# Kernel optimization log

Measured on AMD Instinct MI355X. Metric: run time of the kernel, lower is better.

The kernel has to match this reference:

```python
import jax, jax.numpy as jnp
import numpy as np

N = 50000      # nodes
E = 1600000    # edges (avg degree 32)
DIN, DH, DOUT = 256, 128, 64


def gcn_conv(x, W, b, row, col, w, n):
    """One GCNConv layer (self-loops already appended to row/col/w).
    row = source nodes, col = target nodes; aggregate at targets."""
    xw = x @ W                                        # [n, d_out]
    deg = jax.ops.segment_sum(w, col, num_segments=n)  # in-degree weighted
    dinv = jnp.where(deg > 0, jax.lax.rsqrt(deg), 0.0)
    norm = dinv[row] * w * dinv[col]                  # [E+n]
    msg = norm[:, None] * xw[row]                     # [E+n, d_out] gather
    out = jax.ops.segment_sum(msg, col, num_segments=n)
    return out + b


def setup_inputs() -> dict:
    key = jax.random.key(0)
    k = jax.random.split(key, 6)
    x = jax.random.normal(k[0], (N, DIN), dtype=jnp.float32)
    edge_index = jax.random.randint(k[1], (2, E), 0, N)
    edge_weight = jax.random.uniform(k[2], (E,), dtype=jnp.float32)
    W1 = jax.random.normal(k[3], (DIN, DH), dtype=jnp.float32) * (1.0 / np.sqrt(DIN))
    b1 = jnp.zeros((DH,), dtype=jnp.float32)
    W2 = jax.random.normal(k[4], (DH, DOUT), dtype=jnp.float32) * (1.0 / np.sqrt(DH))
    b2 = jnp.zeros((DOUT,), dtype=jnp.float32)
    return {"x": x, "edge_index": edge_index, "edge_weight": edge_weight,
            "W1": W1, "b1": b1, "W2": W2, "b2": b2}


def reference(x, edge_index, edge_weight, W1, b1, W2, b2):
    n = x.shape[0]
    loops = jnp.arange(n, dtype=edge_index.dtype)
    row = jnp.concatenate([edge_index[0], loops])
    col = jnp.concatenate([edge_index[1], loops])
    w = jnp.concatenate([edge_weight, jnp.ones((n,), dtype=edge_weight.dtype)])
    h = gcn_conv(x, W1, b1, row, col, w, n)
    h = jax.nn.relu(h)
    # dropout(p=0.2) is identity in eval mode
    h = gcn_conv(h, W2, b2, row, col, w, n)
    return jax.nn.log_softmax(h, axis=-1)
```

## Files before the change

kernel.cpp:

```cpp
#include <hip/hip_runtime.h>
#include <hip/hip_bf16.h>
#include <cstddef>


#define DIN 256
#define DH  128
#define DOUT 64
#define NPB 100
#define NBMAX 512

typedef __bf16 bf16x8 __attribute__((ext_vector_type(8)));
typedef float f32x4 __attribute__((ext_vector_type(4)));

__device__ __forceinline__ float bflo(unsigned u) { return __uint_as_float(u << 16); }
__device__ __forceinline__ float bfhi(unsigned u) { return __uint_as_float(u & 0xffff0000u); }
__device__ __forceinline__ unsigned short f2bf(float f) {
    unsigned u = __float_as_uint(f);
    unsigned r = (u + 0x7fffu + ((u >> 16) & 1u)) >> 16;
    return (unsigned short)r;
}

__global__ void prep_w_kernel(const float* __restrict__ W1, const float* __restrict__ W2,
                              unsigned short* __restrict__ wt1, unsigned short* __restrict__ wt2) {
    int i = blockIdx.x * 256 + threadIdx.x;
    if (i < DH * DIN) {
        int nn = i >> 8, k = i & 255;
        wt1[i] = f2bf(W1[k * DH + nn]);
    } else {
        int j = i - DH * DIN;
        if (j < DOUT * DH) {
            int nn = j >> 7, k = j & 127;
            wt2[j] = f2bf(W2[k * DOUT + nn]);
        }
    }
}

__launch_bounds__(256)
__global__ void hist_kernel(const int* __restrict__ col, int* __restrict__ bh,
                            int E, int Ec, int NB) {
    __shared__ int hist[NBMAX];
    int p = blockIdx.x, t = threadIdx.x;
    for (int b = t; b < NB; b += 256) hist[b] = 0;
    __syncthreads();
    int s = p * Ec, e = min(s + Ec, E);
    for (int i = s + t; i < e; i += 256) atomicAdd(&hist[col[i] / NPB], 1);
    __syncthreads();
    for (int b = t; b < NB; b += 256) bh[p * NB + b] = hist[b];
}

__launch_bounds__(512)
__global__ void colscan_kernel(int* __restrict__ bh, int* __restrict__ btotal,
                               int P, int NB) {
    __shared__ int arr[512];
    int b = blockIdx.x, t = threadIdx.x;
    arr[t] = (t < P) ? bh[t * NB + b] : 0;
    __syncthreads();
    for (int off = 1; off < 512; off <<= 1) {
        int v = (t >= off) ? arr[t - off] : 0;
        __syncthreads();
        arr[t] += v;
        __syncthreads();
    }
    int excl = (t == 0) ? 0 : arr[t - 1];
    if (t < P) bh[t * NB + b] = excl;
    if (t == P - 1) btotal[b] = arr[t];
}

__launch_bounds__(512)
__global__ void basescan_kernel(const int* __restrict__ btotal, int* __restrict__ bbase,
                                int* __restrict__ rowptr, int NB, int n, int E) {
    __shared__ int arr[512];
    int t = threadIdx.x;
    arr[t] = (t < NB) ? btotal[t] : 0;
    __syncthreads();
    for (int off = 1; off < 512; off <<= 1) {
        int v = (t >= off) ? arr[t - off] : 0;
        __syncthreads();
        arr[t] += v;
        __syncthreads();
    }
    int excl = (t == 0) ? 0 : arr[t - 1];
    if (t <= NB) bbase[t] = excl;
    if (t == 511) rowptr[n] = E;
}

__launch_bounds__(256)
__global__ void scatter_kernel(const int* __restrict__ row, const int* __restrict__ col,
                               const float* __restrict__ w, const int* __restrict__ bh,
                               const int* __restrict__ bbase, int2* __restrict__ part,
                               int E, int Ec, int NB) {
    __shared__ int cur[NBMAX];
    int p = blockIdx.x, t = threadIdx.x;
    for (int b = t; b < NB; b += 256) cur[b] = bbase[b] + bh[p * NB + b];
    __syncthreads();
    int s = p * Ec, e = min(s + Ec, E);
    for (int i = s + t; i < e; i += 256) {
        int c = col[i];
        int r = row[i];
        int b = c / NPB;
        int pos = atomicAdd(&cur[b], 1);
        part[pos] = make_int2(r | ((c - b * NPB) << 16), __float_as_int(w[i]));
    }
}

__launch_bounds__(256)
__global__ void bucket_csr_kernel(const int2* __restrict__ part, const int* __restrict__ bbase,
                                  float* __restrict__ dinv, int* __restrict__ rowptr,
                                  int2* __restrict__ final_e, int n) {
    __shared__ int   hist[NPB];
    __shared__ float wsum[NPB];
    __shared__ int   nbase[NPB];
    __shared__ int   cur[NPB];
    int b = blockIdx.x, t = threadIdx.x;
    if (t < NPB) { hist[t] = 0; wsum[t] = 0.0f; }
    __syncthreads();
    int s = bbase[b], e = bbase[b + 1];
    for (int i = s + t; i < e; i += 256) {
        int2 rec = part[i];
        int cl = rec.x >> 16;
        atomicAdd(&hist[cl], 1);
        atomicAdd(&wsum[cl], __int_as_float(rec.y));
    }
    __syncthreads();
    if (t == 0) {
        int run = 0;
        for (int k = 0; k < NPB; ++k) { nbase[k] = run; run += hist[k]; }
    }
    __syncthreads();
    if (t < NPB) {
        int node = b * NPB + t;
        if (node < n) {
            dinv[node] = rsqrtf(1.0f + wsum[t]);
            rowptr[node] = s + nbase[t];
        }
        cur[t] = nbase[t];
    }
    __syncthreads();
    for (int i = s + t; i < e; i += 256) {
        int2 rec = part[i];
        int cl = rec.x >> 16;
        int q = s + atomicAdd(&cur[cl], 1);
        final_e[q] = make_int2(rec.x & 0xffff, rec.y);
    }
}

template <int K, int M>
__launch_bounds__(256)
__global__ void gemm_mfma_kernel(const float* __restrict__ A,
                                 const unsigned short* __restrict__ Wt,
                                 const float* __restrict__ scale,
                                 unsigned short* __restrict__ C, int N) {
    constexpr int BK = 64, LD = BK + 8;
    constexpr int WN = M / 4;
    constexpr int NT = WN / 16;
    constexpr int CLD = M + 8;
    constexpr int SM = (64 * LD + M * LD) > (64 * CLD) ? (64 * LD + M * LD) : (64 * CLD);
    __shared__ unsigned short smem[SM];
    __shared__ float sdv[64];
    unsigned short* As = smem;
    unsigned short* Bs = smem + 64 * LD;

    const int tid = threadIdx.x;
    const int row0 = blockIdx.x * 64;
    const int lane = tid & 63;
    const int quad = lane >> 4, r16 = lane & 15;
    const int n0 = (tid >> 6) * WN;

    if (tid < 64) {
        int r = row0 + tid;
        sdv[tid] = (r < N) ? scale[r] : 0.0f;
    }

    f32x4 acc[4][NT];
#pragma unroll
    for (int mt = 0; mt < 4; ++mt)
#pragma unroll
        for (int nt = 0; nt < NT; ++nt)
            acc[mt][nt] = (f32x4){0.f, 0.f, 0.f, 0.f};

    for (int k0 = 0; k0 < K; k0 += BK) {
#pragma unroll
        for (int j = 0; j < 4; ++j) {
            int idx = tid + j * 256;
            int m = idx >> 4;
            int q = idx & 15;
            int gr = row0 + m;
            float4 v = make_float4(0.f, 0.f, 0.f, 0.f);
            if (gr < N) v = *(const float4*)&A[(size_t)gr * K + k0 + q * 4];
            ushort4 s4;
            s4.x = f2bf(v.x); s4.y = f2bf(v.y); s4.z = f2bf(v.z); s4.w = f2bf(v.w);
            *(ushort4*)&As[m * LD + q * 4] = s4;
        }
#pragma unroll
        for (int j = 0; j < M * 8 / 256; ++j) {
            int idx = tid + j * 256;
            int nn = idx >> 3;
            int q = idx & 7;
            uint4 v = *(const uint4*)&Wt[(size_t)nn * K + k0 + q * 8];
            *(uint4*)&Bs[nn * LD + q * 8] = v;
        }
        __syncthreads();
#pragma unroll
        for (int ks = 0; ks < BK / 32; ++ks) {
            bf16x8 af[4], bfr[NT];
#pragma unroll
            for (int nt = 0; nt < NT; ++nt)
                bfr[nt] = *(const bf16x8*)&Bs[(n0 + nt * 16 + r16) * LD + ks * 32 + quad * 8];
#pragma unroll
            for (int mt = 0; mt < 4; ++mt)
                af[mt] = *(const bf16x8*)&As[(mt * 16 + r16) * LD + ks * 32 + quad * 8];
#pragma unroll
            for (int mt = 0; mt < 4; ++mt)
#pragma unroll
                for (int nt = 0; nt < NT; ++nt)
                    acc[mt][nt] = __builtin_amdgcn_mfma_f32_16x16x32_bf16(
                        af[mt], bfr[nt], acc[mt][nt], 0, 0, 0);
        }
        __syncthreads();
    }
    unsigned short* Cs = smem;
#pragma unroll
    for (int mt = 0; mt < 4; ++mt) {
#pragma unroll
        for (int i = 0; i < 4; ++i) {
            int r = mt * 16 + quad * 4 + i;
            float sc = sdv[r];
#pragma unroll
            for (int nt = 0; nt < NT; ++nt)
                Cs[r * CLD + n0 + nt * 16 + r16] = f2bf(acc[mt][nt][i] * sc);
        }
    }
    __syncthreads();
#pragma unroll
    for (int j = 0; j < 64 * M / 8 / 256; ++j) {
        int idx = tid + j * 256;
        int r = idx / (M / 8);
        int q = idx % (M / 8);
        int gr = row0 + r;
        if (gr < N) {
            uint4 v = *(const uint4*)&Cs[r * CLD + q * 8];
            *(uint4*)&C[(size_t)gr * M + q * 8] = v;
        }
    }
}

__launch_bounds__(256)
__global__ void agg1_kernel(const uint2* __restrict__ xw,
                            const int* __restrict__ rowptr,
                            const int2* __restrict__ edge,
                            const float* __restrict__ dinv,
                            const float* __restrict__ bias,
                            float* __restrict__ out, int n) {
    int node = blockIdx.x * 4 + (threadIdx.x >> 6);
    if (node >= n) return;
    int lane = threadIdx.x & 63;
    int half = lane >> 5, sub = lane & 31;
    float a0 = 0.f, a1 = 0.f, a2 = 0.f, a3 = 0.f;
    if (half == 0) {
        uint2 u = xw[(size_t)node * 32 + sub];
        a0 = bflo(u.x); a1 = bfhi(u.x); a2 = bflo(u.y); a3 = bfhi(u.y);
    }
    int p = rowptr[node], p1 = rowptr[node + 1];
    for (; p + 8 <= p1; p += 8) {
        int2 e0 = edge[p + half],     e1 = edge[p + 2 + half];
        int2 e2 = edge[p + 4 + half], e3 = edge[p + 6 + half];
        uint2 v0 = xw[(size_t)e0.x * 32 + sub];
        uint2 v1 = xw[(size_t)e1.x * 32 + sub];
        uint2 v2 = xw[(size_t)e2.x * 32 + sub];
        uint2 v3 = xw[(size_t)e3.x * 32 + sub];
        float w0 = __int_as_float(e0.y), w1 = __int_as_float(e1.y);
        float w2 = __int_as_float(e2.y), w3 = __int_as_float(e3.y);
        a0 += w0 * bflo(v0.x) + w1 * bflo(v1.x) + w2 * bflo(v2.x) + w3 * bflo(v3.x);
        a1 += w0 * bfhi(v0.x) + w1 * bfhi(v1.x) + w2 * bfhi(v2.x) + w3 * bfhi(v3.x);
        a2 += w0 * bflo(v0.y) + w1 * bflo(v1.y) + w2 * bflo(v2.y) + w3 * bflo(v3.y);
        a3 += w0 * bfhi(v0.y) + w1 * bfhi(v1.y) + w2 * bfhi(v2.y) + w3 * bfhi(v3.y);
    }
    for (; p + 2 <= p1; p += 2) {
        int2 e0 = edge[p + half];
        uint2 v0 = xw[(size_t)e0.x * 32 + sub];
        float w0 = __int_as_float(e0.y);
        a0 += w0 * bflo(v0.x); a1 += w0 * bfhi(v0.x);
        a2 += w0 * bflo(v0.y); a3 += w0 * bfhi(v0.y);
    }
    if (p < p1 && half == 0) {
        int2 e0 = edge[p];
        uint2 v0 = xw[(size_t)e0.x * 32 + sub];
        float w0 = __int_as_float(e0.y);
        a0 += w0 * bflo(v0.x); a1 += w0 * bfhi(v0.x);
        a2 += w0 * bflo(v0.y); a3 += w0 * bfhi(v0.y);
    }
    a0 += __shfl_xor(a0, 32); a1 += __shfl_xor(a1, 32);
    a2 += __shfl_xor(a2, 32); a3 += __shfl_xor(a3, 32);
    float di = dinv[node];
    float4 b = ((const float4*)bias)[sub];
    a0 = fmaxf(di * a0 + b.x, 0.f);
    a1 = fmaxf(di * a1 + b.y, 0.f);
    a2 = fmaxf(di * a2 + b.z, 0.f);
    a3 = fmaxf(di * a3 + b.w, 0.f);
    if (half == 0)
        ((float4*)out)[(size_t)node * 32 + sub] = make_float4(a0, a1, a2, a3);
}

__launch_bounds__(256)
__global__ void agg2_kernel(const uint2* __restrict__ xw,
                            const int* __restrict__ rowptr,
                            const int2* __restrict__ edge,
                            const float* __restrict__ dinv,
                            const float* __restrict__ bias,
                            float* __restrict__ out, int n) {
    int node = blockIdx.x * 4 + (threadIdx.x >> 6);
    if (node >= n) return;
    int lane = threadIdx.x & 63;
    int qw = lane >> 4, sub = lane & 15;
    float a0 = 0.f, a1 = 0.f, a2 = 0.f, a3 = 0.f;
    if (qw == 0) {
        uint2 u = xw[(size_t)node * 16 + sub];
        a0 = bflo(u.x); a1 = bfhi(u.x); a2 = bflo(u.y); a3 = bfhi(u.y);
    }
    int p = rowptr[node], p1 = rowptr[node + 1];
    for (; p + 8 <= p1; p += 8) {
        int2 e0 = edge[p + qw], e1 = edge[p + 4 + qw];
        uint2 v0 = xw[(size_t)e0.x * 16 + sub];
        uint2 v1 = xw[(size_t)e1.x * 16 + sub];
        float w0 = __int_as_float(e0.y), w1 = __int_as_float(e1.y);
        a0 += w0 * bflo(v0.x) + w1 * bflo(v1.x);
        a1 += w0 * bfhi(v0.x) + w1 * bfhi(v1.x);
        a2 += w0 * bflo(v0.y) + w1 * bflo(v1.y);
        a3 += w0 * bfhi(v0.y) + w1 * bfhi(v1.y);
    }
    for (; p + 4 <= p1; p += 4) {
        int2 e0 = edge[p + qw];
        uint2 v0 = xw[(size_t)e0.x * 16 + sub];
        float w0 = __int_as_float(e0.y);
        a0 += w0 * bflo(v0.x); a1 += w0 * bfhi(v0.x);
        a2 += w0 * bflo(v0.y); a3 += w0 * bfhi(v0.y);
    }
    int rem = p1 - p;
    if (qw < rem) {
        int2 e0 = edge[p + qw];
        uint2 v0 = xw[(size_t)e0.x * 16 + sub];
        float w0 = __int_as_float(e0.y);
        a0 += w0 * bflo(v0.x); a1 += w0 * bfhi(v0.x);
        a2 += w0 * bflo(v0.y); a3 += w0 * bfhi(v0.y);
    }
    a0 += __shfl_xor(a0, 32); a1 += __shfl_xor(a1, 32);
    a2 += __shfl_xor(a2, 32); a3 += __shfl_xor(a3, 32);
    a0 += __shfl_xor(a0, 16); a1 += __shfl_xor(a1, 16);
    a2 += __shfl_xor(a2, 16); a3 += __shfl_xor(a3, 16);
    float di = dinv[node];
    float4 b = ((const float4*)bias)[sub];
    a0 = di * a0 + b.x; a1 = di * a1 + b.y;
    a2 = di * a2 + b.z; a3 = di * a3 + b.w;
    float m = fmaxf(fmaxf(a0, a1), fmaxf(a2, a3));
#pragma unroll
    for (int off = 8; off > 0; off >>= 1) m = fmaxf(m, __shfl_xor(m, off));
    float s = __expf(a0 - m) + __expf(a1 - m) + __expf(a2 - m) + __expf(a3 - m);
#pragma unroll
    for (int off = 8; off > 0; off >>= 1) s += __shfl_xor(s, off);
    float lse = m + __logf(s);
    if (qw == 0)
        ((float4*)out)[(size_t)node * 16 + sub] =
            make_float4(a0 - lse, a1 - lse, a2 - lse, a3 - lse);
}

extern "C" void kernel_launch(void* const* d_in, const int* in_sizes, int n_in,
                              void* d_out, int out_size, void* d_ws, size_t ws_size,
                              hipStream_t stream) {
    const float* x  = (const float*)d_in[0];
    const int*   ei = (const int*)d_in[1];
    const float* ew = (const float*)d_in[2];
    const float* W1 = (const float*)d_in[3];
    const float* b1 = (const float*)d_in[4];
    const float* W2 = (const float*)d_in[5];
    const float* b2 = (const float*)d_in[6];
    float* out = (float*)d_out;

    const int n = in_sizes[0] / DIN;
    const int E = in_sizes[2];
    const int* row = ei;
    const int* col = ei + E;

    const int NB = (n + NPB - 1) / NPB;
    const int P  = NB;
    const int Ec = (E + P - 1) / P;

    char* ptr = (char*)d_ws;
    auto alloc = [&](size_t bytes) -> void* {
        void* r = (void*)ptr;
        ptr += (bytes + 255) & ~(size_t)255;
        return r;
    };
    int*   bh     = (int*)  alloc((size_t)P * NB * 4);
    int*   btotal = (int*)  alloc((size_t)NB * 4);
    int*   bbase  = (int*)  alloc((size_t)(NB + 1) * 4);
    int*   rowptr = (int*)  alloc((size_t)(n + 1) * 4);
    float* dinv   = (float*)alloc((size_t)n * 4);
    int2*  edge   = (int2*) alloc((size_t)E * 8);
    unsigned short* xw1 = (unsigned short*)alloc((size_t)n * DH * 2);
    unsigned short* wt1 = (unsigned short*)alloc((size_t)DH * DIN * 2);
    unsigned short* wt2 = (unsigned short*)alloc((size_t)DOUT * DH * 2);
    char* tail = (char*)alloc((size_t)n * DH * 4);
    int2*  part = (int2*)tail;
    float* h1   = (float*)tail;
    unsigned short* xw2 = xw1;

    const int nb_g = (n + 63) / 64;
    const int nb_a = (n + 3) / 4;

    prep_w_kernel<<<(DH * DIN + DOUT * DH + 255) / 256, 256, 0, stream>>>(W1, W2, wt1, wt2);
    hist_kernel<<<P, 256, 0, stream>>>(col, bh, E, Ec, NB);
    colscan_kernel<<<NB, 512, 0, stream>>>(bh, btotal, P, NB);
    basescan_kernel<<<1, 512, 0, stream>>>(btotal, bbase, rowptr, NB, n, E);
    scatter_kernel<<<P, 256, 0, stream>>>(row, col, ew, bh, bbase, part, E, Ec, NB);
    bucket_csr_kernel<<<NB, 256, 0, stream>>>(part, bbase, dinv, rowptr, edge, n);

    gemm_mfma_kernel<DIN, DH><<<nb_g, 256, 0, stream>>>(x, wt1, dinv, xw1, n);
    agg1_kernel<<<nb_a, 256, 0, stream>>>((const uint2*)xw1, rowptr, edge, dinv, b1, h1, n);
    gemm_mfma_kernel<DH, DOUT><<<nb_g, 256, 0, stream>>>(h1, wt2, dinv, xw2, n);
    agg2_kernel<<<nb_a, 256, 0, stream>>>((const uint2*)xw2, rowptr, edge, dinv, b2, out, n);
}
```

Measured before the change: 286.6 us.

## Fuse weight prep into histogram, parallel bucket scan, persistent deeper-unrolled aggregation

Merges the weight transpose/bf16 conversion into the histogram kernel as extra blocks, which removes one launch. Replaces the serial single-thread prefix sum in bucket_csr with a block-wide Hillis-Steele scan. Turns both aggregation kernels into grid-stride loops over a fixed 2048-block grid and unrolls the edge loop to 16 edges, so more gathers are in flight per wave. The risks are higher register pressure and some load imbalance from the fixed grid size.

```diff
diff --git a/kernel.cpp b/kernel.cpp
--- a/kernel.cpp
+++ b/kernel.cpp
@@ -20,26 +20,27 @@
     return (unsigned short)r;
 }
 
-__global__ void prep_w_kernel(const float* __restrict__ W1, const float* __restrict__ W2,
-                              unsigned short* __restrict__ wt1, unsigned short* __restrict__ wt2) {
-    int i = blockIdx.x * 256 + threadIdx.x;
-    if (i < DH * DIN) {
-        int nn = i >> 8, k = i & 255;
-        wt1[i] = f2bf(W1[k * DH + nn]);
-    } else {
-        int j = i - DH * DIN;
-        if (j < DOUT * DH) {
-            int nn = j >> 7, k = j & 127;
-            wt2[j] = f2bf(W2[k * DOUT + nn]);
-        }
-    }
-}
-
-__launch_bounds__(256)
-__global__ void hist_kernel(const int* __restrict__ col, int* __restrict__ bh,
-                            int E, int Ec, int NB) {
+__launch_bounds__(256)
+__global__ void hist_prep_kernel(const int* __restrict__ col, int* __restrict__ bh,
+                                 int E, int Ec, int NB, int P,
+                                 const float* __restrict__ W1, const float* __restrict__ W2,
+                                 unsigned short* __restrict__ wt1, unsigned short* __restrict__ wt2) {
     __shared__ int hist[NBMAX];
     int p = blockIdx.x, t = threadIdx.x;
+    if (p >= P) {
+        int i = (p - P) * 256 + t;
+        if (i < DH * DIN) {
+            int nn = i >> 8, k = i & 255;
+            wt1[i] = f2bf(W1[k * DH + nn]);
+        } else {
+            int j = i - DH * DIN;
+            if (j < DOUT * DH) {
+                int nn = j >> 7, k = j & 127;
+                wt2[j] = f2bf(W2[k * DOUT + nn]);
+            }
+        }
+        return;
+    }
     for (int b = t; b < NB; b += 256) hist[b] = 0;
     __syncthreads();
     int s = p * Ec, e = min(s + Ec, E);
@@ -109,6 +110,7 @@
                                   int2* __restrict__ final_e, int n) {
     __shared__ int   hist[NPB];
     __shared__ float wsum[NPB];
+    __shared__ int   arr[256];
     __shared__ int   nbase[NPB];
     __shared__ int   cur[NPB];
     int b = blockIdx.x, t = threadIdx.x;
@@ -122,18 +124,24 @@
         atomicAdd(&wsum[cl], __int_as_float(rec.y));
     }
     __syncthreads();
-    if (t == 0) {
-        int run = 0;
-        for (int k = 0; k < NPB; ++k) { nbase[k] = run; run += hist[k]; }
-    }
-    __syncthreads();
+    int hv = (t < NPB) ? hist[t] : 0;
+    arr[t] = hv;
+    __syncthreads();
+    for (int off = 1; off < 256; off <<= 1) {
+        int v = (t >= off) ? arr[t - off] : 0;
+        __syncthreads();
+        arr[t] += v;
+        __syncthreads();
+    }
     if (t < NPB) {
+        int nb = arr[t] - hv;
+        nbase[t] = nb;
+        cur[t] = nb;
         int node = b * NPB + t;
         if (node < n) {
             dinv[node] = rsqrtf(1.0f + wsum[t]);
-            rowptr[node] = s + nbase[t];
-        }
-        cur[t] = nbase[t];
+            rowptr[node] = s + nb;
+        }
     }
     __syncthreads();
     for (int i = s + t; i < e; i += 256) {
@@ -251,54 +259,55 @@
                             const float* __restrict__ dinv,
                             const float* __restrict__ bias,
                             float* __restrict__ out, int n) {
-    int node = blockIdx.x * 4 + (threadIdx.x >> 6);
-    if (node >= n) return;
-    int lane = threadIdx.x & 63;
-    int half = lane >> 5, sub = lane & 31;
-    float a0 = 0.f, a1 = 0.f, a2 = 0.f, a3 = 0.f;
-    if (half == 0) {
-        uint2 u = xw[(size_t)node * 32 + sub];
-        a0 = bflo(u.x); a1 = bfhi(u.x); a2 = bflo(u.y); a3 = bfhi(u.y);
-    }
-    int p = rowptr[node], p1 = rowptr[node + 1];
-    for (; p + 8 <= p1; p += 8) {
-        int2 e0 = edge[p + half],     e1 = edge[p + 2 + half];
-        int2 e2 = edge[p + 4 + half], e3 = edge[p + 6 + half];
-        uint2 v0 = xw[(size_t)e0.x * 32 + sub];
-        uint2 v1 = xw[(size_t)e1.x * 32 + sub];
-        uint2 v2 = xw[(size_t)e2.x * 32 + sub];
-        uint2 v3 = xw[(size_t)e3.x * 32 + sub];
-        float w0 = __int_as_float(e0.y), w1 = __int_as_float(e1.y);
-        float w2 = __int_as_float(e2.y), w3 = __int_as_float(e3.y);
-        a0 += w0 * bflo(v0.x) + w1 * bflo(v1.x) + w2 * bflo(v2.x) + w3 * bflo(v3.x);
-        a1 += w0 * bfhi(v0.x) + w1 * bfhi(v1.x) + w2 * bfhi(v2.x) + w3 * bfhi(v3.x);
-        a2 += w0 * bflo(v0.y) + w1 * bflo(v1.y) + w2 * bflo(v2.y) + w3 * bflo(v3.y);
-        a3 += w0 * bfhi(v0.y) + w1 * bfhi(v1.y) + w2 * bfhi(v2.y) + w3 * bfhi(v3.y);
-    }
-    for (; p + 2 <= p1; p += 2) {
-        int2 e0 = edge[p + half];
-        uint2 v0 = xw[(size_t)e0.x * 32 + sub];
-        float w0 = __int_as_float(e0.y);
-        a0 += w0 * bflo(v0.x); a1 += w0 * bfhi(v0.x);
-        a2 += w0 * bflo(v0.y); a3 += w0 * bfhi(v0.y);
-    }
-    if (p < p1 && half == 0) {
-        int2 e0 = edge[p];
-        uint2 v0 = xw[(size_t)e0.x * 32 + sub];
-        float w0 = __int_as_float(e0.y);
-        a0 += w0 * bflo(v0.x); a1 += w0 * bfhi(v0.x);
-        a2 += w0 * bflo(v0.y); a3 += w0 * bfhi(v0.y);
-    }
-    a0 += __shfl_xor(a0, 32); a1 += __shfl_xor(a1, 32);
-    a2 += __shfl_xor(a2, 32); a3 += __shfl_xor(a3, 32);
-    float di = dinv[node];
-    float4 b = ((const float4*)bias)[sub];
-    a0 = fmaxf(di * a0 + b.x, 0.f);
-    a1 = fmaxf(di * a1 + b.y, 0.f);
-    a2 = fmaxf(di * a2 + b.z, 0.f);
-    a3 = fmaxf(di * a3 + b.w, 0.f);
-    if (half == 0)
-        ((float4*)out)[(size_t)node * 32 + sub] = make_float4(a0, a1, a2, a3);
+    const int nw = gridDim.x * 4;
+    const int wid = blockIdx.x * 4 + (threadIdx.x >> 6);
+    const int lane = threadIdx.x & 63;
+    const int half = lane >> 5, sub = lane & 31;
+    for (int node = wid; node < n; node += nw) {
+        float a0 = 0.f, a1 = 0.f, a2 = 0.f, a3 = 0.f;
+        if (half == 0) {
+            uint2 u = xw[(size_t)node * 32 + sub];
+            a0 = bflo(u.x); a1 = bfhi(u.x); a2 = bflo(u.y); a3 = bfhi(u.y);
+        }
+        int p = rowptr[node], p1 = rowptr[node + 1];
+        for (; p + 16 <= p1; p += 16) {
+            int2 e[8]; uint2 v[8];
+#pragma unroll
+            for (int j = 0; j < 8; ++j) e[j] = edge[p + 2 * j + half];
+#pragma unroll
+            for (int j = 0; j < 8; ++j) v[j] = xw[(size_t)e[j].x * 32 + sub];
+#pragma unroll
+            for (int j = 0; j < 8; ++j) {
+                float w = __int_as_float(e[j].y);
+                a0 += w * bflo(v[j].x); a1 += w * bfhi(v[j].x);
+                a2 += w * bflo(v[j].y); a3 += w * bfhi(v[j].y);
+            }
+        }
+        for (; p + 2 <= p1; p += 2) {
+            int2 e0 = edge[p + half];
+            uint2 v0 = xw[(size_t)e0.x * 32 + sub];
+            float w0 = __int_as_float(e0.y);
+            a0 += w0 * bflo(v0.x); a1 += w0 * bfhi(v0.x);
+            a2 += w0 * bflo(v0.y); a3 += w0 * bfhi(v0.y);
+        }
+        if (p < p1 && half == 0) {
+            int2 e0 = edge[p];
+            uint2 v0 = xw[(size_t)e0.x * 32 + sub];
+            float w0 = __int_as_float(e0.y);
+            a0 += w0 * bflo(v0.x); a1 += w0 * bfhi(v0.x);
+            a2 += w0 * bflo(v0.y); a3 += w0 * bfhi(v0.y);
+        }
+        a0 += __shfl_xor(a0, 32); a1 += __shfl_xor(a1, 32);
+        a2 += __shfl_xor(a2, 32); a3 += __shfl_xor(a3, 32);
+        float di = dinv[node];
+        float4 b = ((const float4*)bias)[sub];
+        a0 = fmaxf(di * a0 + b.x, 0.f);
+        a1 = fmaxf(di * a1 + b.y, 0.f);
+        a2 = fmaxf(di * a2 + b.z, 0.f);
+        a3 = fmaxf(di * a3 + b.w, 0.f);
+        if (half == 0)
+            ((float4*)out)[(size_t)node * 32 + sub] = make_float4(a0, a1, a2, a3);
+    }
 }
 
 __launch_bounds__(256)
@@ -308,59 +317,64 @@
                             const float* __restrict__ dinv,
                             const float* __restrict__ bias,
                             float* __restrict__ out, int n) {
-    int node = blockIdx.x * 4 + (threadIdx.x >> 6);
-    if (node >= n) return;
-    int lane = threadIdx.x & 63;
-    int qw = lane >> 4, sub = lane & 15;
-    float a0 = 0.f, a1 = 0.f, a2 = 0.f, a3 = 0.f;
-    if (qw == 0) {
-        uint2 u = xw[(size_t)node * 16 + sub];
-        a0 = bflo(u.x); a1 = bfhi(u.x); a2 = bflo(u.y); a3 = bfhi(u.y);
-    }
-    int p = rowptr[node], p1 = rowptr[node + 1];
-    for (; p + 8 <= p1; p += 8) {
-        int2 e0 = edge[p + qw], e1 = edge[p + 4 + qw];
-        uint2 v0 = xw[(size_t)e0.x * 16 + sub];
-        uint2 v1 = xw[(size_t)e1.x * 16 + sub];
-        float w0 = __int_as_float(e0.y), w1 = __int_as_float(e1.y);
-        a0 += w0 * bflo(v0.x) + w1 * bflo(v1.x);
-        a1 += w0 * bfhi(v0.x) + w1 * bfhi(v1.x);
-        a2 += w0 * bflo(v0.y) + w1 * bflo(v1.y);
-        a3 += w0 * bfhi(v0.y) + w1 * bfhi(v1.y);
-    }
-    for (; p + 4 <= p1; p += 4) {
-        int2 e0 = edge[p + qw];
-        uint2 v0 = xw[(size_t)e0.x * 16 + sub];
-        float w0 = __int_as_float(e0.y);
-        a0 += w0 * bflo(v0.x); a1 += w0 * bfhi(v0.x);
-        a2 += w0 * bflo(v0.y); a3 += w0 * bfhi(v0.y);
-    }
-    int rem = p1 - p;
-    if (qw < rem) {
-        int2 e0 = edge[p + qw];
-        uint2 v0 = xw[(size_t)e0.x * 16 + sub];
-        float w0 = __int_as_float(e0.y);
-        a0 += w0 * bflo(v0.x); a1 += w0 * bfhi(v0.x);
-        a2 += w0 * bflo(v0.y); a3 += w0 * bfhi(v0.y);
-    }
-    a0 += __shfl_xor(a0, 32); a1 += __shfl_xor(a1, 32);
-    a2 += __shfl_xor(a2, 32); a3 += __shfl_xor(a3, 32);
-    a0 += __shfl_xor(a0, 16); a1 += __shfl_xor(a1, 16);
-    a2 += __shfl_xor(a2, 16); a3 += __shfl_xor(a3, 16);
-    float di = dinv[node];
-    float4 b = ((const float4*)bias)[sub];
-    a0 = di * a0 + b.x; a1 = di * a1 + b.y;
-    a2 = di * a2 + b.z; a3 = di * a3 + b.w;
-    float m = fmaxf(fmaxf(a0, a1), fmaxf(a2, a3));
-#pragma unroll
-    for (int off = 8; off > 0; off >>= 1) m = fmaxf(m, __shfl_xor(m, off));
-    float s = __expf(a0 - m) + __expf(a1 - m) + __expf(a2 - m) + __expf(a3 - m);
-#pragma unroll
-    for (int off = 8; off > 0; off >>= 1) s += __shfl_xor(s, off);
-    float lse = m + __logf(s);
-    if (qw == 0)
-        ((float4*)out)[(size_t)node * 16 + sub] =
-            make_float4(a0 - lse, a1 - lse, a2 - lse, a3 - lse);
+    const int nw = gridDim.x * 4;
+    const int wid = blockIdx.x * 4 + (threadIdx.x >> 6);
+    const int lane = threadIdx.x & 63;
+    const int qw = lane >> 4, sub = lane & 15;
+    for (int node = wid; node < n; node += nw) {
+        float a0 = 0.f, a1 = 0.f, a2 = 0.f, a3 = 0.f;
+        if (qw == 0) {
+            uint2 u = xw[(size_t)node * 16 + sub];
+            a0 = bflo(u.x); a1 = bfhi(u.x); a2 = bflo(u.y); a3 = bfhi(u.y);
+        }
+        int p = rowptr[node], p1 = rowptr[node + 1];
+        for (; p + 16 <= p1; p += 16) {
+            int2 e[4]; uint2 v[4];
+#pragma unroll
+            for (int j = 0; j < 4; ++j) e[j] = edge[p + 4 * j + qw];
+#pragma unroll
+            for (int j = 0; j < 4; ++j) v[j] = xw[(size_t)e[j].x * 16 + sub];
+#pragma unroll
+            for (int j = 0; j < 4; ++j) {
+                float w = __int_as_float(e[j].y);
+                a0 += w * bflo(v[j].x); a1 += w * bfhi(v[j].x);
+                a2 += w * bflo(v[j].y); a3 += w * bfhi(v[j].y);
+            }
+        }
+        for (; p + 4 <= p1; p += 4) {
+            int2 e0 = edge[p + qw];
+            uint2 v0 = xw[(size_t)e0.x * 16 + sub];
+            float w0 = __int_as_float(e0.y);
+            a0 += w0 * bflo(v0.x); a1 += w0 * bfhi(v0.x);
+            a2 += w0 * bflo(v0.y); a3 += w0 * bfhi(v0.y);
+        }
+        int rem = p1 - p;
+        if (qw < rem) {
+            int2 e0 = edge[p + qw];
+            uint2 v0 = xw[(size_t)e0.x * 16 + sub];
+            float w0 = __int_as_float(e0.y);
+            a0 += w0 * bflo(v0.x); a1 += w0 * bfhi(v0.x);
+            a2 += w0 * bflo(v0.y); a3 += w0 * bfhi(v0.y);
+        }
+        a0 += __shfl_xor(a0, 32); a1 += __shfl_xor(a1, 32);
+        a2 += __shfl_xor(a2, 32); a3 += __shfl_xor(a3, 32);
+        a0 += __shfl_xor(a0, 16); a1 += __shfl_xor(a1, 16);
+        a2 += __shfl_xor(a2, 16); a3 += __shfl_xor(a3, 16);
+        float di = dinv[node];
+        float4 b = ((const float4*)bias)[sub];
+        a0 = di * a0 + b.x; a1 = di * a1 + b.y;
+        a2 = di * a2 + b.z; a3 = di * a3 + b.w;
+        float m = fmaxf(fmaxf(a0, a1), fmaxf(a2, a3));
+#pragma unroll
+        for (int off = 8; off > 0; off >>= 1) m = fmaxf(m, __shfl_xor(m, off));
+        float s = __expf(a0 - m) + __expf(a1 - m) + __expf(a2 - m) + __expf(a3 - m);
+#pragma unroll
+        for (int off = 8; off > 0; off >>= 1) s += __shfl_xor(s, off);
+        float lse = m + __logf(s);
+        if (qw == 0)
+            ((float4*)out)[(size_t)node * 16 + sub] =
+                make_float4(a0 - lse, a1 - lse, a2 - lse, a3 - lse);
+    }
 }
 
 extern "C" void kernel_launch(void* const* d_in, const int* in_sizes, int n_in,
@@ -405,17 +419,17 @@
     unsigned short* xw2 = xw1;
 
     const int nb_g = (n + 63) / 64;
-    const int nb_a = (n + 3) / 4;
-
-    prep_w_kernel<<<(DH * DIN + DOUT * DH + 255) / 256, 256, 0, stream>>>(W1, W2, wt1, wt2);
-    hist_kernel<<<P, 256, 0, stream>>>(col, bh, E, Ec, NB);
+    const int nb_agg = 2048;
+    const int PREPB = (DH * DIN + DOUT * DH + 255) / 256;
+
+    hist_prep_kernel<<<P + PREPB, 256, 0, stream>>>(col, bh, E, Ec, NB, P, W1, W2, wt1, wt2);
     colscan_kernel<<<NB, 512, 0, stream>>>(bh, btotal, P, NB);
     basescan_kernel<<<1, 512, 0, stream>>>(btotal, bbase, rowptr, NB, n, E);
     scatter_kernel<<<P, 256, 0, stream>>>(row, col, ew, bh, bbase, part, E, Ec, NB);
     bucket_csr_kernel<<<NB, 256, 0, stream>>>(part, bbase, dinv, rowptr, edge, n);
 
     gemm_mfma_kernel<DIN, DH><<<nb_g, 256, 0, stream>>>(x, wt1, dinv, xw1, n);
-    agg1_kernel<<<nb_a, 256, 0, stream>>>((const uint2*)xw1, rowptr, edge, dinv, b1, h1, n);
+    agg1_kernel<<<nb_agg, 256, 0, stream>>>((const uint2*)xw1, rowptr, edge, dinv, b1, h1, n);
     gemm_mfma_kernel<DH, DOUT><<<nb_g, 256, 0, stream>>>(h1, wt2, dinv, xw2, n);
-    agg2_kernel<<<nb_a, 256, 0, stream>>>((const uint2*)xw2, rowptr, edge, dinv, b2, out, n);
-}
+    agg2_kernel<<<nb_agg, 256, 0, stream>>>((const uint2*)xw2, rowptr, edge, dinv, b2, out, n);
+}
```

Result: slower. 311.3 us (+8.6%).
